# Optimization experiments

Measured on AMD Instinct MI355X. Metric: run time of the kernel, lower is better.

## Reference

```python
import jax, jax.numpy as jnp
import numpy as np

B = 16          # number of point clouds in the batch
N_COARSE = 1024 # coarse points per cloud
N_FINE = 4096   # fine (skip) points per cloud
C_IN = 256
C_SKIP = 128
K = 3
EPS = 1e-16


def setup_inputs() -> dict:
    key = jax.random.key(0)
    ks = jax.random.split(key, 8)
    x = jax.random.normal(ks[0], (B * N_COARSE, C_IN), dtype=jnp.float32)
    pos = jax.random.uniform(ks[1], (B * N_COARSE, 3), dtype=jnp.float32)
    x_skip = jax.random.normal(ks[2], (B * N_FINE, C_SKIP), dtype=jnp.float32)
    pos_skip = jax.random.uniform(ks[3], (B * N_FINE, 3), dtype=jnp.float32)
    batch = jnp.repeat(jnp.arange(B, dtype=jnp.int64), N_COARSE)
    batch_skip = jnp.repeat(jnp.arange(B, dtype=jnp.int64), N_FINE)
    W1 = jax.random.normal(ks[4], (C_IN + C_SKIP, 256), dtype=jnp.float32) * (1.0 / np.sqrt(C_IN + C_SKIP))
    b1 = jnp.zeros((256,), dtype=jnp.float32)
    W2 = jax.random.normal(ks[5], (256, 256), dtype=jnp.float32) * (1.0 / np.sqrt(256))
    b2 = jnp.zeros((256,), dtype=jnp.float32)
    return {"x": x, "pos": pos, "batch": batch, "x_skip": x_skip,
            "pos_skip": pos_skip, "batch_skip": batch_skip,
            "W1": W1, "b1": b1, "W2": W2, "b2": b2}


def _knn_interpolate(x, pos, pos_skip):
    # Equal-sized clouds: reshape to [B, N, *] and do batched kNN.
    xc = x.reshape(B, N_COARSE, C_IN)
    pc = pos.reshape(B, N_COARSE, 3)
    pf = pos_skip.reshape(B, N_FINE, 3)
    # squared pairwise distances [B, M, N]
    d2 = (jnp.sum(pf * pf, -1)[:, :, None]
          + jnp.sum(pc * pc, -1)[:, None, :]
          - 2.0 * jnp.einsum('bmd,bnd->bmn', pf, pc))
    d2 = jnp.maximum(d2, 0.0)
    neg_d2k, idx = jax.lax.top_k(-d2, K)          # k smallest distances
    w = 1.0 / jnp.maximum(-neg_d2k, EPS)          # [B, M, K] inverse-sq-dist weights
    gathered = jax.vmap(lambda f, i: f[i])(xc, idx)  # [B, M, K, C]
    y = jnp.sum(w[..., None] * gathered, axis=2) / jnp.sum(w, axis=2, keepdims=True)
    return y.reshape(B * N_FINE, C_IN)


def reference(x, pos, batch, x_skip, pos_skip, batch_skip, W1, b1, W2, b2):
    x_interp = _knn_interpolate(x, pos, pos_skip)          # [B*M, C_IN]
    h = jnp.concatenate([x_interp, x_skip], axis=1)        # [B*M, C_IN + C_SKIP]
    h = jax.nn.relu(h @ W1 + b1)
    out = jax.nn.relu(h @ W2 + b2)
    return out
```

## Files before the change

### kernel.cpp

```cpp
#include <hip/hip_runtime.h>

typedef float  f32x4  __attribute__((ext_vector_type(4)));
typedef short  short8 __attribute__((ext_vector_type(8)));
typedef unsigned short ushort_t;
typedef ushort_t us4   __attribute__((ext_vector_type(4)));

#define NCOARSE 1024
#define NFINE   4096

__device__ __forceinline__ ushort_t f2bf(float f){
  union { float f; unsigned u; } a; a.f = f;
  unsigned u = a.u;
  return (ushort_t)((u + 0x7fffu + ((u >> 16) & 1u)) >> 16);
}

__device__ __forceinline__ f32x4 splat4(float v){ f32x4 t = {v, v, v, v}; return t; }

__global__ void prep_w(const float* __restrict__ W, ushort_t* __restrict__ Wp, int nelem){
  int e = blockIdx.x * 256 + threadIdx.x;
  if (e >= nelem) return;
  int j    = e & 7;
  int lane = (e >> 3) & 63;
  int g    = e >> 9;
  int nb   = g & 15;
  int kc   = g >> 4;
  int k = kc * 32 + (lane >> 4) * 8 + j;
  int n = nb * 16 + (lane & 15);
  Wp[e] = f2bf(W[k * 256 + n]);
}

__global__ __launch_bounds__(256) void knn_kernel(const float* __restrict__ pos,
                           const float* __restrict__ pos_skip,
                           int* __restrict__ knn_i, float* __restrict__ knn_w){
  __shared__ f32x4 cand[8][129];
  const int tid = threadIdx.x;
  const int b   = blockIdx.x >> 7;
  const int m   = blockIdx.x * 32 + (tid >> 3);
  const int chunk = tid & 7;

  const float* p = pos + (size_t)b * NCOARSE * 3;
  for (int c = tid; c < NCOARSE; c += 256){
    float x = p[3*c], y = p[3*c+1], z = p[3*c+2];
    float sc = __fadd_rn(__fadd_rn(__fmul_rn(x,x), __fmul_rn(y,y)), __fmul_rn(z,z));
    f32x4 v = { x, y, z, sc };
    cand[c >> 7][c & 127] = v;
  }
  __syncthreads();

  const float* q = pos_skip + (size_t)m * 3;
  float qx = q[0], qy = q[1], qz = q[2];
  float sf = __fadd_rn(__fadd_rn(__fmul_rn(qx,qx), __fmul_rn(qy,qy)), __fmul_rn(qz,qz));

  float d0 = 1e30f, d1 = 1e30f, d2 = 1e30f;
  int   i0 = 0,     i1 = 0,     i2 = 0;
  const int gbase = chunk * 128;
  #pragma unroll 4
  for (int i = 0; i < 128; ++i){
    f32x4 v = cand[chunk][i];
    float dot = __fadd_rn(__fadd_rn(__fmul_rn(qx, v.x), __fmul_rn(qy, v.y)),
                          __fmul_rn(qz, v.z));
    float d = __fsub_rn(__fadd_rn(sf, v.w), __fmul_rn(2.0f, dot));
    d = fmaxf(d, 0.0f);
    if (d < d2){
      int gi = gbase + i;
      if (d < d1){
        d2 = d1; i2 = i1;
        if (d < d0){ d1 = d0; i1 = i0; d0 = d; i0 = gi; }
        else       { d1 = d;  i1 = gi; }
      } else { d2 = d; i2 = gi; }
    }
  }

  #pragma unroll
  for (int mlev = 1; mlev <= 4; mlev <<= 1){
    float e0 = __shfl_xor(d0, mlev), e1 = __shfl_xor(d1, mlev), e2 = __shfl_xor(d2, mlev);
    int   j0 = __shfl_xor(i0, mlev), j1 = __shfl_xor(i1, mlev), j2 = __shfl_xor(i2, mlev);
    #pragma unroll
    for (int s = 0; s < 3; ++s){
      float e = (s == 0) ? e0 : (s == 1) ? e1 : e2;
      int   j = (s == 0) ? j0 : (s == 1) ? j1 : j2;
      bool l2 = (e < d2) || (e == d2 && j < i2);
      if (l2){
        bool l1 = (e < d1) || (e == d1 && j < i1);
        if (l1){
          d2 = d1; i2 = i1;
          bool l0 = (e < d0) || (e == d0 && j < i0);
          if (l0){ d1 = d0; i1 = i0; d0 = e; i0 = j; }
          else   { d1 = e;  i1 = j; }
        } else { d2 = e; i2 = j; }
      }
    }
  }

  if (chunk == 0){
    float w0 = 1.0f / fmaxf(d0, 1e-16f);
    float w1 = 1.0f / fmaxf(d1, 1e-16f);
    float w2 = 1.0f / fmaxf(d2, 1e-16f);
    float ws = __fadd_rn(__fadd_rn(w0, w1), w2);
    knn_i[3*m]   = b * NCOARSE + i0;
    knn_i[3*m+1] = b * NCOARSE + i1;
    knn_i[3*m+2] = b * NCOARSE + i2;
    knn_w[3*m]   = w0 / ws;
    knn_w[3*m+1] = w1 / ws;
    knn_w[3*m+2] = w2 / ws;
  }
}

__global__ __launch_bounds__(256, 4)
void fused_fp(const float* __restrict__ x, const float* __restrict__ x_skip,
              const int* __restrict__ knn_i, const float* __restrict__ knn_w,
              const ushort_t* __restrict__ W1p, const float* __restrict__ b1,
              const ushort_t* __restrict__ W2p, const float* __restrict__ b2,
              float* __restrict__ out){
  __shared__ ushort_t hbuf[32 * 384];
  char* h1b = (char*)hbuf;
  char* h2b = (char*)hbuf;
  const int tid  = threadIdx.x;
  const int lb   = ((blockIdx.x & 7) << 8) + (blockIdx.x >> 3);
  const int row0 = lb * 32;
  const int wp   = tid >> 6;
  const int lane = tid & 63;
  const int lhi  = lane >> 4;
  const int llo  = lane & 15;

  {
    const int r   = tid >> 3;
    const int sub = tid & 7;
    const int m   = row0 + r;
    const f32x4* xsr = (const f32x4*)(x_skip + (size_t)m * 128);
    f32x4 xs[4];
    #pragma unroll
    for (int it = 0; it < 4; ++it) xs[it] = xsr[it * 8 + sub];
    int i0 = knn_i[3*m], i1 = knn_i[3*m+1], i2 = knn_i[3*m+2];
    float w0 = knn_w[3*m], w1 = knn_w[3*m+1], w2 = knn_w[3*m+2];
    const f32x4* x0 = (const f32x4*)(x + (size_t)i0 * 256);
    const f32x4* x1 = (const f32x4*)(x + (size_t)i1 * 256);
    const f32x4* x2 = (const f32x4*)(x + (size_t)i2 * 256);
    #pragma unroll
    for (int it = 0; it < 8; ++it){
      int c4 = it * 8 + sub;
      f32x4 v = x0[c4] * w0 + x1[c4] * w1 + x2[c4] * w2;
      int byte = (r * 768 + c4 * 8) ^ ((r & 7) << 4);
      us4 pk = { f2bf(v.x), f2bf(v.y), f2bf(v.z), f2bf(v.w) };
      *(us4*)(h1b + byte) = pk;
    }
    #pragma unroll
    for (int it = 0; it < 4; ++it){
      int c4 = it * 8 + sub;
      f32x4 v = xs[it];
      int byte = (r * 768 + 512 + c4 * 8) ^ ((r & 7) << 4);
      us4 pk = { f2bf(v.x), f2bf(v.y), f2bf(v.z), f2bf(v.w) };
      *(us4*)(h1b + byte) = pk;
    }
  }
  __syncthreads();

  f32x4 acc[2][4];
  #pragma unroll
  for (int nbp = 0; nbp < 4; ++nbp){
    float bb = b1[wp * 64 + nbp * 16 + llo];
    #pragma unroll
    for (int mb = 0; mb < 2; ++mb) acc[mb][nbp] = splat4(bb);
  }
  #pragma unroll
  for (int kk = 0; kk < 12; ++kk){
    short8 af[2];
    #pragma unroll
    for (int mb = 0; mb < 2; ++mb){
      int r = mb * 16 + llo;
      int byte = (r * 768 + kk * 64 + lhi * 16) ^ ((r & 7) << 4);
      af[mb] = *(const short8*)(h1b + byte);
    }
    short8 bfr[4];
    #pragma unroll
    for (int nbp = 0; nbp < 4; ++nbp)
      bfr[nbp] = *(const short8*)(W1p + ((size_t)((kk * 16 + wp * 4 + nbp) * 64 + lane)) * 8);
    #pragma unroll
    for (int mb = 0; mb < 2; ++mb)
      #pragma unroll
      for (int nbp = 0; nbp < 4; ++nbp)
        acc[mb][nbp] = __builtin_amdgcn_mfma_f32_16x16x32_bf16(af[mb], bfr[nbp], acc[mb][nbp], 0, 0, 0);
  }
  __syncthreads();

  #pragma unroll
  for (int mb = 0; mb < 2; ++mb)
    #pragma unroll
    for (int nbp = 0; nbp < 4; ++nbp)
      #pragma unroll
      for (int rg = 0; rg < 4; ++rg){
        int r   = mb * 16 + lhi * 4 + rg;
        int col = wp * 64 + nbp * 16 + llo;
        int byte = (r * 512 + col * 2) ^ ((r & 7) << 4);
        *(ushort_t*)(h2b + byte) = f2bf(fmaxf(acc[mb][nbp][rg], 0.0f));
      }
  __syncthreads();

  f32x4 acc2[2][4];
  #pragma unroll
  for (int nbp = 0; nbp < 4; ++nbp){
    float bb = b2[wp * 64 + nbp * 16 + llo];
    #pragma unroll
    for (int mb = 0; mb < 2; ++mb) acc2[mb][nbp] = splat4(bb);
  }
  #pragma unroll
  for (int kk = 0; kk < 8; ++kk){
    short8 af[2];
    #pragma unroll
    for (int mb = 0; mb < 2; ++mb){
      int r = mb * 16 + llo;
      int byte = (r * 512 + kk * 64 + lhi * 16) ^ ((r & 7) << 4);
      af[mb] = *(const short8*)(h2b + byte);
    }
    short8 bfr[4];
    #pragma unroll
    for (int nbp = 0; nbp < 4; ++nbp)
      bfr[nbp] = *(const short8*)(W2p + ((size_t)((kk * 16 + wp * 4 + nbp) * 64 + lane)) * 8);
    #pragma unroll
    for (int mb = 0; mb < 2; ++mb)
      #pragma unroll
      for (int nbp = 0; nbp < 4; ++nbp)
        acc2[mb][nbp] = __builtin_amdgcn_mfma_f32_16x16x32_bf16(af[mb], bfr[nbp], acc2[mb][nbp], 0, 0, 0);
  }

  #pragma unroll
  for (int mb = 0; mb < 2; ++mb)
    #pragma unroll
    for (int nbp = 0; nbp < 4; ++nbp)
      #pragma unroll
      for (int rg = 0; rg < 4; ++rg){
        int row = row0 + mb * 16 + lhi * 4 + rg;
        int col = wp * 64 + nbp * 16 + llo;
        out[(size_t)row * 256 + col] = fmaxf(acc2[mb][nbp][rg], 0.0f);
      }
}

extern "C" void kernel_launch(void* const* d_in, const int* in_sizes, int n_in,
                              void* d_out, int out_size, void* d_ws, size_t ws_size,
                              hipStream_t stream){
  (void)in_sizes; (void)n_in; (void)out_size; (void)ws_size;
  const float* x        = (const float*)d_in[0];
  const float* pos      = (const float*)d_in[1];
  const float* x_skip   = (const float*)d_in[3];
  const float* pos_skip = (const float*)d_in[4];
  const float* W1 = (const float*)d_in[6];
  const float* b1 = (const float*)d_in[7];
  const float* W2 = (const float*)d_in[8];
  const float* b2 = (const float*)d_in[9];
  float* out = (float*)d_out;
  char* ws = (char*)d_ws;
  ushort_t* W1p = (ushort_t*)(ws);
  ushort_t* W2p = (ushort_t*)(ws + 196608);
  int*      ki  = (int*)(ws + 327680);
  float*    kw  = (float*)(ws + 1114112);

  hipLaunchKernelGGL(prep_w, dim3(384), dim3(256), 0, stream, W1, W1p, 98304);
  hipLaunchKernelGGL(prep_w, dim3(256), dim3(256), 0, stream, W2, W2p, 65536);
  hipLaunchKernelGGL(knn_kernel, dim3(2048), dim3(256), 0, stream, pos, pos_skip, ki, kw);
  hipLaunchKernelGGL(fused_fp, dim3(2048), dim3(256), 0, stream,
                     x, x_skip, ki, kw, W1p, b1, W2p, b2, out);
}
```

Measured before the change: 87.91 us.

## Split fused MLP into two persistent GEMM kernels with register-resident weights

Replaces the single fused kernel with two kernels of 512 threads that each process four 32-row tiles. Each wave keeps its slice of W1 or W2 in registers for the whole block instead of reloading weight fragments from global memory per tile. The intermediate activation is written to a workspace buffer in bf16, already in MFMA fragment layout, and read back by the second GEMM. In exchange this adds an extra global round-trip for the hidden layer and one more launch, and the large register weight arrays may lower occupancy.

```diff
diff --git a/kernel.cpp b/kernel.cpp
--- a/kernel.cpp
+++ b/kernel.cpp
@@ -106,133 +106,161 @@
   }
 }
 
-__global__ __launch_bounds__(256, 4)
-void fused_fp(const float* __restrict__ x, const float* __restrict__ x_skip,
+__global__ __launch_bounds__(512, 4)
+void gemm1_fp(const float* __restrict__ x, const float* __restrict__ x_skip,
               const int* __restrict__ knn_i, const float* __restrict__ knn_w,
               const ushort_t* __restrict__ W1p, const float* __restrict__ b1,
-              const ushort_t* __restrict__ W2p, const float* __restrict__ b2,
-              float* __restrict__ out){
-  __shared__ ushort_t hbuf[32 * 384];
-  char* h1b = (char*)hbuf;
-  char* h2b = (char*)hbuf;
+              ushort_t* __restrict__ h2p){
+  __shared__ ushort_t h1[32 * 384];
+  __shared__ ushort_t h2[32 * 256];
+  char* h1b = (char*)h1;
+  char* h2b = (char*)h2;
   const int tid  = threadIdx.x;
-  const int lb   = ((blockIdx.x & 7) << 8) + (blockIdx.x >> 3);
-  const int row0 = lb * 32;
-  const int wp   = tid >> 6;
+  const int lb   = ((blockIdx.x & 7) << 6) + (blockIdx.x >> 3);
+  const int wq   = tid >> 6;
   const int lane = tid & 63;
   const int lhi  = lane >> 4;
   const int llo  = lane & 15;
 
-  {
-    const int r   = tid >> 3;
-    const int sub = tid & 7;
-    const int m   = row0 + r;
-    const f32x4* xsr = (const f32x4*)(x_skip + (size_t)m * 128);
-    f32x4 xs[4];
-    #pragma unroll
-    for (int it = 0; it < 4; ++it) xs[it] = xsr[it * 8 + sub];
-    int i0 = knn_i[3*m], i1 = knn_i[3*m+1], i2 = knn_i[3*m+2];
-    float w0 = knn_w[3*m], w1 = knn_w[3*m+1], w2 = knn_w[3*m+2];
-    const f32x4* x0 = (const f32x4*)(x + (size_t)i0 * 256);
-    const f32x4* x1 = (const f32x4*)(x + (size_t)i1 * 256);
-    const f32x4* x2 = (const f32x4*)(x + (size_t)i2 * 256);
-    #pragma unroll
-    for (int it = 0; it < 8; ++it){
-      int c4 = it * 8 + sub;
-      f32x4 v = x0[c4] * w0 + x1[c4] * w1 + x2[c4] * w2;
-      int byte = (r * 768 + c4 * 8) ^ ((r & 7) << 4);
-      us4 pk = { f2bf(v.x), f2bf(v.y), f2bf(v.z), f2bf(v.w) };
-      *(us4*)(h1b + byte) = pk;
-    }
-    #pragma unroll
-    for (int it = 0; it < 4; ++it){
-      int c4 = it * 8 + sub;
-      f32x4 v = xs[it];
-      int byte = (r * 768 + 512 + c4 * 8) ^ ((r & 7) << 4);
-      us4 pk = { f2bf(v.x), f2bf(v.y), f2bf(v.z), f2bf(v.w) };
-      *(us4*)(h1b + byte) = pk;
-    }
-  }
-  __syncthreads();
-
-  f32x4 acc[2][4];
+  short8 wfr[12][2];
   #pragma unroll
-  for (int nbp = 0; nbp < 4; ++nbp){
-    float bb = b1[wp * 64 + nbp * 16 + llo];
-    #pragma unroll
-    for (int mb = 0; mb < 2; ++mb) acc[mb][nbp] = splat4(bb);
-  }
+  for (int kk = 0; kk < 12; ++kk)
+    #pragma unroll
+    for (int nbp = 0; nbp < 2; ++nbp)
+      wfr[kk][nbp] = *(const short8*)(W1p + ((size_t)((kk * 16 + wq * 2 + nbp) * 64 + lane)) * 8);
+  const float bb0 = b1[wq * 32 + llo];
+  const float bb1 = b1[wq * 32 + 16 + llo];
+
+  const int r   = tid >> 4;
+  const int sub = tid & 15;
+
+  for (int t = 0; t < 4; ++t){
+    const int g    = lb * 4 + t;
+    const int row0 = g * 32;
+
+    {
+      const int m = row0 + r;
+      int i0 = knn_i[3*m], i1 = knn_i[3*m+1], i2 = knn_i[3*m+2];
+      float w0 = knn_w[3*m], w1 = knn_w[3*m+1], w2 = knn_w[3*m+2];
+      const f32x4* x0 = (const f32x4*)(x + (size_t)i0 * 256);
+      const f32x4* x1 = (const f32x4*)(x + (size_t)i1 * 256);
+      const f32x4* x2 = (const f32x4*)(x + (size_t)i2 * 256);
+      #pragma unroll
+      for (int it = 0; it < 4; ++it){
+        int c4 = it * 16 + sub;
+        f32x4 v = x0[c4] * w0 + x1[c4] * w1 + x2[c4] * w2;
+        int byte = (r * 768 + c4 * 8) ^ ((r & 7) << 4);
+        us4 pk = { f2bf(v.x), f2bf(v.y), f2bf(v.z), f2bf(v.w) };
+        *(us4*)(h1b + byte) = pk;
+      }
+      const f32x4* xs = (const f32x4*)(x_skip + (size_t)m * 128);
+      #pragma unroll
+      for (int it = 0; it < 2; ++it){
+        int c4 = it * 16 + sub;
+        f32x4 v = xs[c4];
+        int byte = (r * 768 + 512 + c4 * 8) ^ ((r & 7) << 4);
+        us4 pk = { f2bf(v.x), f2bf(v.y), f2bf(v.z), f2bf(v.w) };
+        *(us4*)(h1b + byte) = pk;
+      }
+    }
+    __syncthreads();
+
+    f32x4 acc[2][2];
+    acc[0][0] = splat4(bb0); acc[1][0] = splat4(bb0);
+    acc[0][1] = splat4(bb1); acc[1][1] = splat4(bb1);
+    #pragma unroll
+    for (int kk = 0; kk < 12; ++kk){
+      short8 af[2];
+      #pragma unroll
+      for (int mb = 0; mb < 2; ++mb){
+        int rr = mb * 16 + llo;
+        int byte = (rr * 768 + kk * 64 + lhi * 16) ^ ((rr & 7) << 4);
+        af[mb] = *(const short8*)(h1b + byte);
+      }
+      #pragma unroll
+      for (int mb = 0; mb < 2; ++mb)
+        #pragma unroll
+        for (int nbp = 0; nbp < 2; ++nbp)
+          acc[mb][nbp] = __builtin_amdgcn_mfma_f32_16x16x32_bf16(af[mb], wfr[kk][nbp], acc[mb][nbp], 0, 0, 0);
+    }
+
+    #pragma unroll
+    for (int mb = 0; mb < 2; ++mb)
+      #pragma unroll
+      for (int nbp = 0; nbp < 2; ++nbp)
+        #pragma unroll
+        for (int rg = 0; rg < 4; ++rg){
+          int rr  = mb * 16 + lhi * 4 + rg;
+          int col = wq * 32 + nbp * 16 + llo;
+          int byte = (rr * 512 + col * 2) ^ ((rr & 7) << 4);
+          *(ushort_t*)(h2b + byte) = f2bf(fmaxf(acc[mb][nbp][rg], 0.0f));
+        }
+    __syncthreads();
+
+    #pragma unroll
+    for (int ss = 0; ss < 2; ++ss){
+      int s   = tid * 2 + ss;
+      int fa  = s >> 6;
+      int l   = s & 63;
+      int kk2 = fa >> 1;
+      int mb2 = fa & 1;
+      int row = mb2 * 16 + (l & 15);
+      int byte = (row * 512 + kk2 * 64 + (l >> 4) * 16) ^ ((row & 7) << 4);
+      short8 v = *(const short8*)(h2b + byte);
+      *(short8*)(h2p + ((size_t)(g * 16 + fa) * 64 + l) * 8) = v;
+    }
+  }
+}
+
+__global__ __launch_bounds__(512, 4)
+void gemm2_fp(const ushort_t* __restrict__ h2p,
+              const ushort_t* __restrict__ W2p, const float* __restrict__ b2,
+              float* __restrict__ out){
+  const int tid  = threadIdx.x;
+  const int lb   = ((blockIdx.x & 7) << 6) + (blockIdx.x >> 3);
+  const int wq   = tid >> 6;
+  const int lane = tid & 63;
+  const int lhi  = lane >> 4;
+  const int llo  = lane & 15;
+
+  short8 wfr[8][2];
   #pragma unroll
-  for (int kk = 0; kk < 12; ++kk){
-    short8 af[2];
-    #pragma unroll
-    for (int mb = 0; mb < 2; ++mb){
-      int r = mb * 16 + llo;
-      int byte = (r * 768 + kk * 64 + lhi * 16) ^ ((r & 7) << 4);
-      af[mb] = *(const short8*)(h1b + byte);
-    }
-    short8 bfr[4];
-    #pragma unroll
-    for (int nbp = 0; nbp < 4; ++nbp)
-      bfr[nbp] = *(const short8*)(W1p + ((size_t)((kk * 16 + wp * 4 + nbp) * 64 + lane)) * 8);
+  for (int kk = 0; kk < 8; ++kk)
+    #pragma unroll
+    for (int nbp = 0; nbp < 2; ++nbp)
+      wfr[kk][nbp] = *(const short8*)(W2p + ((size_t)((kk * 16 + wq * 2 + nbp) * 64 + lane)) * 8);
+  const float bb0 = b2[wq * 32 + llo];
+  const float bb1 = b2[wq * 32 + 16 + llo];
+
+  for (int t = 0; t < 4; ++t){
+    const int g    = lb * 4 + t;
+    const int row0 = g * 32;
+
+    f32x4 acc[2][2];
+    acc[0][0] = splat4(bb0); acc[1][0] = splat4(bb0);
+    acc[0][1] = splat4(bb1); acc[1][1] = splat4(bb1);
+    #pragma unroll
+    for (int kk = 0; kk < 8; ++kk){
+      short8 a0 = *(const short8*)(h2p + ((size_t)(g * 16 + kk * 2 + 0) * 64 + lane) * 8);
+      short8 a1 = *(const short8*)(h2p + ((size_t)(g * 16 + kk * 2 + 1) * 64 + lane) * 8);
+      #pragma unroll
+      for (int nbp = 0; nbp < 2; ++nbp){
+        acc[0][nbp] = __builtin_amdgcn_mfma_f32_16x16x32_bf16(a0, wfr[kk][nbp], acc[0][nbp], 0, 0, 0);
+        acc[1][nbp] = __builtin_amdgcn_mfma_f32_16x16x32_bf16(a1, wfr[kk][nbp], acc[1][nbp], 0, 0, 0);
+      }
+    }
+
     #pragma unroll
     for (int mb = 0; mb < 2; ++mb)
       #pragma unroll
-      for (int nbp = 0; nbp < 4; ++nbp)
-        acc[mb][nbp] = __builtin_amdgcn_mfma_f32_16x16x32_bf16(af[mb], bfr[nbp], acc[mb][nbp], 0, 0, 0);
-  }
-  __syncthreads();
-
-  #pragma unroll
-  for (int mb = 0; mb < 2; ++mb)
-    #pragma unroll
-    for (int nbp = 0; nbp < 4; ++nbp)
-      #pragma unroll
-      for (int rg = 0; rg < 4; ++rg){
-        int r   = mb * 16 + lhi * 4 + rg;
-        int col = wp * 64 + nbp * 16 + llo;
-        int byte = (r * 512 + col * 2) ^ ((r & 7) << 4);
-        *(ushort_t*)(h2b + byte) = f2bf(fmaxf(acc[mb][nbp][rg], 0.0f));
-      }
-  __syncthreads();
-
-  f32x4 acc2[2][4];
-  #pragma unroll
-  for (int nbp = 0; nbp < 4; ++nbp){
-    float bb = b2[wp * 64 + nbp * 16 + llo];
-    #pragma unroll
-    for (int mb = 0; mb < 2; ++mb) acc2[mb][nbp] = splat4(bb);
-  }
-  #pragma unroll
-  for (int kk = 0; kk < 8; ++kk){
-    short8 af[2];
-    #pragma unroll
-    for (int mb = 0; mb < 2; ++mb){
-      int r = mb * 16 + llo;
-      int byte = (r * 512 + kk * 64 + lhi * 16) ^ ((r & 7) << 4);
-      af[mb] = *(const short8*)(h2b + byte);
-    }
-    short8 bfr[4];
-    #pragma unroll
-    for (int nbp = 0; nbp < 4; ++nbp)
-      bfr[nbp] = *(const short8*)(W2p + ((size_t)((kk * 16 + wp * 4 + nbp) * 64 + lane)) * 8);
-    #pragma unroll
-    for (int mb = 0; mb < 2; ++mb)
-      #pragma unroll
-      for (int nbp = 0; nbp < 4; ++nbp)
-        acc2[mb][nbp] = __builtin_amdgcn_mfma_f32_16x16x32_bf16(af[mb], bfr[nbp], acc2[mb][nbp], 0, 0, 0);
-  }
-
-  #pragma unroll
-  for (int mb = 0; mb < 2; ++mb)
-    #pragma unroll
-    for (int nbp = 0; nbp < 4; ++nbp)
-      #pragma unroll
-      for (int rg = 0; rg < 4; ++rg){
-        int row = row0 + mb * 16 + lhi * 4 + rg;
-        int col = wp * 64 + nbp * 16 + llo;
-        out[(size_t)row * 256 + col] = fmaxf(acc2[mb][nbp][rg], 0.0f);
-      }
+      for (int nbp = 0; nbp < 2; ++nbp)
+        #pragma unroll
+        for (int rg = 0; rg < 4; ++rg){
+          int row = row0 + mb * 16 + lhi * 4 + rg;
+          int col = wq * 32 + nbp * 16 + llo;
+          out[(size_t)row * 256 + col] = fmaxf(acc[mb][nbp][rg], 0.0f);
+        }
+  }
 }
 
 extern "C" void kernel_launch(void* const* d_in, const int* in_sizes, int n_in,
@@ -253,10 +281,13 @@
   ushort_t* W2p = (ushort_t*)(ws + 196608);
   int*      ki  = (int*)(ws + 327680);
   float*    kw  = (float*)(ws + 1114112);
+  ushort_t* h2p = (ushort_t*)(ws + 1900544);
 
   hipLaunchKernelGGL(prep_w, dim3(384), dim3(256), 0, stream, W1, W1p, 98304);
   hipLaunchKernelGGL(prep_w, dim3(256), dim3(256), 0, stream, W2, W2p, 65536);
   hipLaunchKernelGGL(knn_kernel, dim3(2048), dim3(256), 0, stream, pos, pos_skip, ki, kw);
-  hipLaunchKernelGGL(fused_fp, dim3(2048), dim3(256), 0, stream,
-                     x, x_skip, ki, kw, W1p, b1, W2p, b2, out);
-}
+  hipLaunchKernelGGL(gemm1_fp, dim3(512), dim3(512), 0, stream,
+                     x, x_skip, ki, kw, W1p, b1, h2p);
+  hipLaunchKernelGGL(gemm2_fp, dim3(512), dim3(512), 0, stream,
+                     h2p, W2p, b2, out);
+}
```

Result: slower. 170.6 us (+94.1%).

## Process two queries per thread in kNN and prefetch weight fragments in MLP

Applied to the files above, without the earlier changes.

The kNN kernel now has each thread handle two fine query points against the same shared-memory candidate chunk. This halves the grid and amortises the LDS candidate loads and the per-block candidate setup. The fused MLP kernel keeps a three-deep register ring of weight fragments, loading the fragments for step kk+3 while the MFMAs for step kk run, to hide global/L2 latency. Launch bounds drop to 3 blocks per SM to make room for the extra registers, which lowers occupancy.

```diff
diff --git a/kernel.cpp b/kernel.cpp
--- a/kernel.cpp
+++ b/kernel.cpp
@@ -34,8 +34,9 @@
                            int* __restrict__ knn_i, float* __restrict__ knn_w){
   __shared__ f32x4 cand[8][129];
   const int tid = threadIdx.x;
-  const int b   = blockIdx.x >> 7;
-  const int m   = blockIdx.x * 32 + (tid >> 3);
+  const int b   = blockIdx.x >> 6;
+  const int mA  = blockIdx.x * 64 + (tid >> 3);
+  const int mB  = mA + 32;
   const int chunk = tid & 7;
 
   const float* p = pos + (size_t)b * NCOARSE * 3;
@@ -47,66 +48,117 @@
   }
   __syncthreads();
 
-  const float* q = pos_skip + (size_t)m * 3;
-  float qx = q[0], qy = q[1], qz = q[2];
-  float sf = __fadd_rn(__fadd_rn(__fmul_rn(qx,qx), __fmul_rn(qy,qy)), __fmul_rn(qz,qz));
-
-  float d0 = 1e30f, d1 = 1e30f, d2 = 1e30f;
-  int   i0 = 0,     i1 = 0,     i2 = 0;
+  const float* qA = pos_skip + (size_t)mA * 3;
+  const float* qB = pos_skip + (size_t)mB * 3;
+  float ax = qA[0], ay = qA[1], az = qA[2];
+  float bx = qB[0], by = qB[1], bz = qB[2];
+  float sfA = __fadd_rn(__fadd_rn(__fmul_rn(ax,ax), __fmul_rn(ay,ay)), __fmul_rn(az,az));
+  float sfB = __fadd_rn(__fadd_rn(__fmul_rn(bx,bx), __fmul_rn(by,by)), __fmul_rn(bz,bz));
+
+  float dA0 = 1e30f, dA1 = 1e30f, dA2 = 1e30f;
+  int   iA0 = 0,     iA1 = 0,     iA2 = 0;
+  float dB0 = 1e30f, dB1 = 1e30f, dB2 = 1e30f;
+  int   iB0 = 0,     iB1 = 0,     iB2 = 0;
   const int gbase = chunk * 128;
-  #pragma unroll 4
+  #pragma unroll 2
   for (int i = 0; i < 128; ++i){
     f32x4 v = cand[chunk][i];
-    float dot = __fadd_rn(__fadd_rn(__fmul_rn(qx, v.x), __fmul_rn(qy, v.y)),
-                          __fmul_rn(qz, v.z));
-    float d = __fsub_rn(__fadd_rn(sf, v.w), __fmul_rn(2.0f, dot));
-    d = fmaxf(d, 0.0f);
-    if (d < d2){
-      int gi = gbase + i;
-      if (d < d1){
-        d2 = d1; i2 = i1;
-        if (d < d0){ d1 = d0; i1 = i0; d0 = d; i0 = gi; }
-        else       { d1 = d;  i1 = gi; }
-      } else { d2 = d; i2 = gi; }
+    int gi = gbase + i;
+    float dotA = __fadd_rn(__fadd_rn(__fmul_rn(ax, v.x), __fmul_rn(ay, v.y)),
+                           __fmul_rn(az, v.z));
+    float dA = fmaxf(__fsub_rn(__fadd_rn(sfA, v.w), __fmul_rn(2.0f, dotA)), 0.0f);
+    if (dA < dA2){
+      if (dA < dA1){
+        dA2 = dA1; iA2 = iA1;
+        if (dA < dA0){ dA1 = dA0; iA1 = iA0; dA0 = dA; iA0 = gi; }
+        else         { dA1 = dA;  iA1 = gi; }
+      } else { dA2 = dA; iA2 = gi; }
+    }
+    float dotB = __fadd_rn(__fadd_rn(__fmul_rn(bx, v.x), __fmul_rn(by, v.y)),
+                           __fmul_rn(bz, v.z));
+    float dB = fmaxf(__fsub_rn(__fadd_rn(sfB, v.w), __fmul_rn(2.0f, dotB)), 0.0f);
+    if (dB < dB2){
+      if (dB < dB1){
+        dB2 = dB1; iB2 = iB1;
+        if (dB < dB0){ dB1 = dB0; iB1 = iB0; dB0 = dB; iB0 = gi; }
+        else         { dB1 = dB;  iB1 = gi; }
+      } else { dB2 = dB; iB2 = gi; }
     }
   }
 
   #pragma unroll
   for (int mlev = 1; mlev <= 4; mlev <<= 1){
-    float e0 = __shfl_xor(d0, mlev), e1 = __shfl_xor(d1, mlev), e2 = __shfl_xor(d2, mlev);
-    int   j0 = __shfl_xor(i0, mlev), j1 = __shfl_xor(i1, mlev), j2 = __shfl_xor(i2, mlev);
+    float e0 = __shfl_xor(dA0, mlev), e1 = __shfl_xor(dA1, mlev), e2 = __shfl_xor(dA2, mlev);
+    int   j0 = __shfl_xor(iA0, mlev), j1 = __shfl_xor(iA1, mlev), j2 = __shfl_xor(iA2, mlev);
     #pragma unroll
     for (int s = 0; s < 3; ++s){
       float e = (s == 0) ? e0 : (s == 1) ? e1 : e2;
       int   j = (s == 0) ? j0 : (s == 1) ? j1 : j2;
-      bool l2 = (e < d2) || (e == d2 && j < i2);
+      bool l2 = (e < dA2) || (e == dA2 && j < iA2);
       if (l2){
-        bool l1 = (e < d1) || (e == d1 && j < i1);
+        bool l1 = (e < dA1) || (e == dA1 && j < iA1);
         if (l1){
-          d2 = d1; i2 = i1;
-          bool l0 = (e < d0) || (e == d0 && j < i0);
-          if (l0){ d1 = d0; i1 = i0; d0 = e; i0 = j; }
-          else   { d1 = e;  i1 = j; }
-        } else { d2 = e; i2 = j; }
+          dA2 = dA1; iA2 = iA1;
+          bool l0 = (e < dA0) || (e == dA0 && j < iA0);
+          if (l0){ dA1 = dA0; iA1 = iA0; dA0 = e; iA0 = j; }
+          else   { dA1 = e;  iA1 = j; }
+        } else { dA2 = e; iA2 = j; }
+      }
+    }
+    float f0 = __shfl_xor(dB0, mlev), f1 = __shfl_xor(dB1, mlev), f2 = __shfl_xor(dB2, mlev);
+    int   k0 = __shfl_xor(iB0, mlev), k1 = __shfl_xor(iB1, mlev), k2 = __shfl_xor(iB2, mlev);
+    #pragma unroll
+    for (int s = 0; s < 3; ++s){
+      float e = (s == 0) ? f0 : (s == 1) ? f1 : f2;
+      int   j = (s == 0) ? k0 : (s == 1) ? k1 : k2;
+      bool l2 = (e < dB2) || (e == dB2 && j < iB2);
+      if (l2){
+        bool l1 = (e < dB1) || (e == dB1 && j < iB1);
+        if (l1){
+          dB2 = dB1; iB2 = iB1;
+          bool l0 = (e < dB0) || (e == dB0 && j < iB0);
+          if (l0){ dB1 = dB0; iB1 = iB0; dB0 = e; iB0 = j; }
+          else   { dB1 = e;  iB1 = j; }
+        } else { dB2 = e; iB2 = j; }
       }
     }
   }
 
   if (chunk == 0){
-    float w0 = 1.0f / fmaxf(d0, 1e-16f);
-    float w1 = 1.0f / fmaxf(d1, 1e-16f);
-    float w2 = 1.0f / fmaxf(d2, 1e-16f);
-    float ws = __fadd_rn(__fadd_rn(w0, w1), w2);
-    knn_i[3*m]   = b * NCOARSE + i0;
-    knn_i[3*m+1] = b * NCOARSE + i1;
-    knn_i[3*m+2] = b * NCOARSE + i2;
-    knn_w[3*m]   = w0 / ws;
-    knn_w[3*m+1] = w1 / ws;
-    knn_w[3*m+2] = w2 / ws;
-  }
-}
-
-__global__ __launch_bounds__(256, 4)
+    {
+      float w0 = 1.0f / fmaxf(dA0, 1e-16f);
+      float w1 = 1.0f / fmaxf(dA1, 1e-16f);
+      float w2 = 1.0f / fmaxf(dA2, 1e-16f);
+      float ws = __fadd_rn(__fadd_rn(w0, w1), w2);
+      knn_i[3*mA]   = b * NCOARSE + iA0;
+      knn_i[3*mA+1] = b * NCOARSE + iA1;
+      knn_i[3*mA+2] = b * NCOARSE + iA2;
+      knn_w[3*mA]   = w0 / ws;
+      knn_w[3*mA+1] = w1 / ws;
+      knn_w[3*mA+2] = w2 / ws;
+    }
+    {
+      float w0 = 1.0f / fmaxf(dB0, 1e-16f);
+      float w1 = 1.0f / fmaxf(dB1, 1e-16f);
+      float w2 = 1.0f / fmaxf(dB2, 1e-16f);
+      float ws = __fadd_rn(__fadd_rn(w0, w1), w2);
+      knn_i[3*mB]   = b * NCOARSE + iB0;
+      knn_i[3*mB+1] = b * NCOARSE + iB1;
+      knn_i[3*mB+2] = b * NCOARSE + iB2;
+      knn_w[3*mB]   = w0 / ws;
+      knn_w[3*mB+1] = w1 / ws;
+      knn_w[3*mB+2] = w2 / ws;
+    }
+  }
+}
+
+#define LDW4(DST, WP, STEP)                                                   \
+  { _Pragma("unroll")                                                         \
+    for (int n_ = 0; n_ < 4; ++n_)                                            \
+      DST[n_] = *(const short8*)((WP) +                                       \
+          ((size_t)(((STEP) * 16 + wp * 4 + n_) * 64 + lane)) * 8); }
+
+__global__ __launch_bounds__(256, 3)
 void fused_fp(const float* __restrict__ x, const float* __restrict__ x_skip,
               const int* __restrict__ knn_i, const float* __restrict__ knn_w,
               const ushort_t* __restrict__ W1p, const float* __restrict__ b1,
@@ -162,36 +214,40 @@
     #pragma unroll
     for (int mb = 0; mb < 2; ++mb) acc[mb][nbp] = splat4(bb);
   }
-  #pragma unroll
-  for (int kk = 0; kk < 12; ++kk){
-    short8 af[2];
-    #pragma unroll
-    for (int mb = 0; mb < 2; ++mb){
-      int r = mb * 16 + llo;
-      int byte = (r * 768 + kk * 64 + lhi * 16) ^ ((r & 7) << 4);
-      af[mb] = *(const short8*)(h1b + byte);
-    }
-    short8 bfr[4];
+  {
+    short8 wr[3][4];
+    LDW4(wr[0], W1p, 0);
+    LDW4(wr[1], W1p, 1);
+    LDW4(wr[2], W1p, 2);
+    #pragma unroll
+    for (int kk = 0; kk < 12; ++kk){
+      short8 af[2];
+      #pragma unroll
+      for (int mb = 0; mb < 2; ++mb){
+        int rr = mb * 16 + llo;
+        int byte = (rr * 768 + kk * 64 + lhi * 16) ^ ((rr & 7) << 4);
+        af[mb] = *(const short8*)(h1b + byte);
+      }
+      #pragma unroll
+      for (int mb = 0; mb < 2; ++mb)
+        #pragma unroll
+        for (int nbp = 0; nbp < 4; ++nbp)
+          acc[mb][nbp] = __builtin_amdgcn_mfma_f32_16x16x32_bf16(
+              af[mb], wr[kk % 3][nbp], acc[mb][nbp], 0, 0, 0);
+      if (kk + 3 < 12) { LDW4(wr[kk % 3], W1p, kk + 3); }
+    }
+  }
+  __syncthreads();
+
+  #pragma unroll
+  for (int mb = 0; mb < 2; ++mb)
     #pragma unroll
     for (int nbp = 0; nbp < 4; ++nbp)
-      bfr[nbp] = *(const short8*)(W1p + ((size_t)((kk * 16 + wp * 4 + nbp) * 64 + lane)) * 8);
-    #pragma unroll
-    for (int mb = 0; mb < 2; ++mb)
-      #pragma unroll
-      for (int nbp = 0; nbp < 4; ++nbp)
-        acc[mb][nbp] = __builtin_amdgcn_mfma_f32_16x16x32_bf16(af[mb], bfr[nbp], acc[mb][nbp], 0, 0, 0);
-  }
-  __syncthreads();
-
-  #pragma unroll
-  for (int mb = 0; mb < 2; ++mb)
-    #pragma unroll
-    for (int nbp = 0; nbp < 4; ++nbp)
       #pragma unroll
       for (int rg = 0; rg < 4; ++rg){
-        int r   = mb * 16 + lhi * 4 + rg;
+        int rr  = mb * 16 + lhi * 4 + rg;
         int col = wp * 64 + nbp * 16 + llo;
-        int byte = (r * 512 + col * 2) ^ ((r & 7) << 4);
+        int byte = (rr * 512 + col * 2) ^ ((rr & 7) << 4);
         *(ushort_t*)(h2b + byte) = f2bf(fmaxf(acc[mb][nbp][rg], 0.0f));
       }
   __syncthreads();
@@ -203,24 +259,28 @@
     #pragma unroll
     for (int mb = 0; mb < 2; ++mb) acc2[mb][nbp] = splat4(bb);
   }
-  #pragma unroll
-  for (int kk = 0; kk < 8; ++kk){
-    short8 af[2];
-    #pragma unroll
-    for (int mb = 0; mb < 2; ++mb){
-      int r = mb * 16 + llo;
-      int byte = (r * 512 + kk * 64 + lhi * 16) ^ ((r & 7) << 4);
-      af[mb] = *(const short8*)(h2b + byte);
-    }
-    short8 bfr[4];
-    #pragma unroll
-    for (int nbp = 0; nbp < 4; ++nbp)
-      bfr[nbp] = *(const short8*)(W2p + ((size_t)((kk * 16 + wp * 4 + nbp) * 64 + lane)) * 8);
-    #pragma unroll
-    for (int mb = 0; mb < 2; ++mb)
-      #pragma unroll
-      for (int nbp = 0; nbp < 4; ++nbp)
-        acc2[mb][nbp] = __builtin_amdgcn_mfma_f32_16x16x32_bf16(af[mb], bfr[nbp], acc2[mb][nbp], 0, 0, 0);
+  {
+    short8 wr[3][4];
+    LDW4(wr[0], W2p, 0);
+    LDW4(wr[1], W2p, 1);
+    LDW4(wr[2], W2p, 2);
+    #pragma unroll
+    for (int kk = 0; kk < 8; ++kk){
+      short8 af[2];
+      #pragma unroll
+      for (int mb = 0; mb < 2; ++mb){
+        int rr = mb * 16 + llo;
+        int byte = (rr * 512 + kk * 64 + lhi * 16) ^ ((rr & 7) << 4);
+        af[mb] = *(const short8*)(h2b + byte);
+      }
+      #pragma unroll
+      for (int mb = 0; mb < 2; ++mb)
+        #pragma unroll
+        for (int nbp = 0; nbp < 4; ++nbp)
+          acc2[mb][nbp] = __builtin_amdgcn_mfma_f32_16x16x32_bf16(
+              af[mb], wr[kk % 3][nbp], acc2[mb][nbp], 0, 0, 0);
+      if (kk + 3 < 8) { LDW4(wr[kk % 3], W2p, kk + 3); }
+    }
   }
 
   #pragma unroll
@@ -256,7 +316,7 @@
 
   hipLaunchKernelGGL(prep_w, dim3(384), dim3(256), 0, stream, W1, W1p, 98304);
   hipLaunchKernelGGL(prep_w, dim3(256), dim3(256), 0, stream, W2, W2p, 65536);
-  hipLaunchKernelGGL(knn_kernel, dim3(2048), dim3(256), 0, stream, pos, pos_skip, ki, kw);
+  hipLaunchKernelGGL(knn_kernel, dim3(1024), dim3(256), 0, stream, pos, pos_skip, ki, kw);
   hipLaunchKernelGGL(fused_fp, dim3(2048), dim3(256), 0, stream,
                      x, x_skip, ki, kw, W1p, b1, W2p, b2, out);
 }
```

Result: slower. 93.10 us (+5.9%).

## Prefetch MLP weight fragments into LDS with a triple-buffered async pipeline

Applied to the files above, without the earlier changes.

The fused MLP kernel no longer reads bf16 weight fragments from global memory right before each MFMA step. It now streams them into a three-slot LDS ring with global_load_lds, two k-steps ahead, using vmcnt waits and a barrier on every step. The goal is to hide weight-load latency behind the matrix math. The two weight-prep kernels are merged into one launch, and the occupancy hint drops from 4 to 2 blocks per SM. The extra 48KB of LDS and the per-step barriers lower occupancy and may cost more than the latency they hide, and no fragment is shared across waves.

```diff
diff --git a/kernel.cpp b/kernel.cpp
--- a/kernel.cpp
+++ b/kernel.cpp
@@ -8,6 +8,11 @@
 #define NCOARSE 1024
 #define NFINE   4096
 
+#define GLL16(g, l)                                                   \
+  __builtin_amdgcn_global_load_lds(                                   \
+      (__attribute__((address_space(1))) void*)(g),                   \
+      (__attribute__((address_space(3))) void*)(l), 16, 0, 0)
+
 __device__ __forceinline__ ushort_t f2bf(float f){
   union { float f; unsigned u; } a; a.f = f;
   unsigned u = a.u;
@@ -16,17 +21,20 @@
 
 __device__ __forceinline__ f32x4 splat4(float v){ f32x4 t = {v, v, v, v}; return t; }
 
-__global__ void prep_w(const float* __restrict__ W, ushort_t* __restrict__ Wp, int nelem){
+__global__ void prep_w2(const float* __restrict__ W1, const float* __restrict__ W2,
+                        ushort_t* __restrict__ W1p, ushort_t* __restrict__ W2p){
   int e = blockIdx.x * 256 + threadIdx.x;
-  if (e >= nelem) return;
-  int j    = e & 7;
-  int lane = (e >> 3) & 63;
-  int g    = e >> 9;
+  const float* W; ushort_t* Wp; int idx;
+  if (e < 98304){ W = W1; Wp = W1p; idx = e; }
+  else          { W = W2; Wp = W2p; idx = e - 98304; }
+  int j    = idx & 7;
+  int lane = (idx >> 3) & 63;
+  int g    = idx >> 9;
   int nb   = g & 15;
   int kc   = g >> 4;
   int k = kc * 32 + (lane >> 4) * 8 + j;
   int n = nb * 16 + (lane & 15);
-  Wp[e] = f2bf(W[k * 256 + n]);
+  Wp[idx] = f2bf(W[k * 256 + n]);
 }
 
 __global__ __launch_bounds__(256) void knn_kernel(const float* __restrict__ pos,
@@ -106,13 +114,14 @@
   }
 }
 
-__global__ __launch_bounds__(256, 4)
+__global__ __launch_bounds__(256, 2)
 void fused_fp(const float* __restrict__ x, const float* __restrict__ x_skip,
               const int* __restrict__ knn_i, const float* __restrict__ knn_w,
               const ushort_t* __restrict__ W1p, const float* __restrict__ b1,
               const ushort_t* __restrict__ W2p, const float* __restrict__ b2,
               float* __restrict__ out){
-  __shared__ ushort_t hbuf[32 * 384];
+  __shared__ __align__(16) ushort_t hbuf[32 * 384];
+  __shared__ __align__(16) ushort_t wbuf[3][8192];
   char* h1b = (char*)hbuf;
   char* h2b = (char*)hbuf;
   const int tid  = threadIdx.x;
@@ -123,6 +132,20 @@
   const int lhi  = lane >> 4;
   const int llo  = lane & 15;
 
+  auto stageW = [&](int s){
+    const ushort_t* Wsel = (s < 12) ? W1p : W2p;
+    int fbase = ((s < 12) ? s : (s - 12)) * 16 + wp * 4;
+    #pragma unroll
+    for (int i = 0; i < 4; ++i){
+      const ushort_t* g = Wsel + (size_t)(fbase + i) * 512 + lane * 8;
+      ushort_t* l = &wbuf[s % 3][(wp * 4 + i) * 512];
+      GLL16(g, l);
+    }
+  };
+
+  stageW(0);
+  stageW(1);
+
   {
     const int r   = tid >> 3;
     const int sub = tid & 7;
@@ -164,22 +187,27 @@
   }
   #pragma unroll
   for (int kk = 0; kk < 12; ++kk){
+    asm volatile("s_waitcnt vmcnt(4)" ::: "memory");
+    __builtin_amdgcn_s_barrier();
+    asm volatile("" ::: "memory");
+    stageW(kk + 2);
     short8 af[2];
     #pragma unroll
     for (int mb = 0; mb < 2; ++mb){
-      int r = mb * 16 + llo;
-      int byte = (r * 768 + kk * 64 + lhi * 16) ^ ((r & 7) << 4);
+      int rr = mb * 16 + llo;
+      int byte = (rr * 768 + kk * 64 + lhi * 16) ^ ((rr & 7) << 4);
       af[mb] = *(const short8*)(h1b + byte);
     }
-    short8 bfr[4];
-    #pragma unroll
-    for (int nbp = 0; nbp < 4; ++nbp)
-      bfr[nbp] = *(const short8*)(W1p + ((size_t)((kk * 16 + wp * 4 + nbp) * 64 + lane)) * 8);
+    short8 wf[4];
+    #pragma unroll
+    for (int nbp = 0; nbp < 4; ++nbp)
+      wf[nbp] = *(const short8*)&wbuf[kk % 3][(wp * 4 + nbp) * 512 + lane * 8];
     #pragma unroll
     for (int mb = 0; mb < 2; ++mb)
       #pragma unroll
       for (int nbp = 0; nbp < 4; ++nbp)
-        acc[mb][nbp] = __builtin_amdgcn_mfma_f32_16x16x32_bf16(af[mb], bfr[nbp], acc[mb][nbp], 0, 0, 0);
+        acc[mb][nbp] = __builtin_amdgcn_mfma_f32_16x16x32_bf16(
+            af[mb], wf[nbp], acc[mb][nbp], 0, 0, 0);
   }
   __syncthreads();
 
@@ -189,9 +217,9 @@
     for (int nbp = 0; nbp < 4; ++nbp)
       #pragma unroll
       for (int rg = 0; rg < 4; ++rg){
-        int r   = mb * 16 + lhi * 4 + rg;
+        int rr  = mb * 16 + lhi * 4 + rg;
         int col = wp * 64 + nbp * 16 + llo;
-        int byte = (r * 512 + col * 2) ^ ((r & 7) << 4);
+        int byte = (rr * 512 + col * 2) ^ ((rr & 7) << 4);
         *(ushort_t*)(h2b + byte) = f2bf(fmaxf(acc[mb][nbp][rg], 0.0f));
       }
   __syncthreads();
@@ -204,23 +232,30 @@
     for (int mb = 0; mb < 2; ++mb) acc2[mb][nbp] = splat4(bb);
   }
   #pragma unroll
-  for (int kk = 0; kk < 8; ++kk){
+  for (int t = 0; t < 8; ++t){
+    const int s = 12 + t;
+    if (t < 7) { asm volatile("s_waitcnt vmcnt(4)" ::: "memory"); }
+    else       { asm volatile("s_waitcnt vmcnt(0)" ::: "memory"); }
+    __builtin_amdgcn_s_barrier();
+    asm volatile("" ::: "memory");
+    if (t < 6) stageW(s + 2);
     short8 af[2];
     #pragma unroll
     for (int mb = 0; mb < 2; ++mb){
-      int r = mb * 16 + llo;
-      int byte = (r * 512 + kk * 64 + lhi * 16) ^ ((r & 7) << 4);
+      int rr = mb * 16 + llo;
+      int byte = (rr * 512 + t * 64 + lhi * 16) ^ ((rr & 7) << 4);
       af[mb] = *(const short8*)(h2b + byte);
     }
-    short8 bfr[4];
-    #pragma unroll
-    for (int nbp = 0; nbp < 4; ++nbp)
-      bfr[nbp] = *(const short8*)(W2p + ((size_t)((kk * 16 + wp * 4 + nbp) * 64 + lane)) * 8);
+    short8 wf[4];
+    #pragma unroll
+    for (int nbp = 0; nbp < 4; ++nbp)
+      wf[nbp] = *(const short8*)&wbuf[s % 3][(wp * 4 + nbp) * 512 + lane * 8];
     #pragma unroll
     for (int mb = 0; mb < 2; ++mb)
       #pragma unroll
       for (int nbp = 0; nbp < 4; ++nbp)
-        acc2[mb][nbp] = __builtin_amdgcn_mfma_f32_16x16x32_bf16(af[mb], bfr[nbp], acc2[mb][nbp], 0, 0, 0);
+        acc2[mb][nbp] = __builtin_amdgcn_mfma_f32_16x16x32_bf16(
+            af[mb], wf[nbp], acc2[mb][nbp], 0, 0, 0);
   }
 
   #pragma unroll
@@ -254,8 +289,7 @@
   int*      ki  = (int*)(ws + 327680);
   float*    kw  = (float*)(ws + 1114112);
 
-  hipLaunchKernelGGL(prep_w, dim3(384), dim3(256), 0, stream, W1, W1p, 98304);
-  hipLaunchKernelGGL(prep_w, dim3(256), dim3(256), 0, stream, W2, W2p, 65536);
+  hipLaunchKernelGGL(prep_w2, dim3(640), dim3(256), 0, stream, W1, W2, W1p, W2p);
   hipLaunchKernelGGL(knn_kernel, dim3(2048), dim3(256), 0, stream, pos, pos_skip, ki, kw);
   hipLaunchKernelGGL(fused_fp, dim3(2048), dim3(256), 0, stream,
                      x, x_skip, ki, kw, W1p, b1, W2p, b2, out);
```

New measurement: 96.09 us. 1.09x slower.
